# Performance work log

Measured on AMD Instinct MI355X. Metric: run time of the kernel, lower is better.

## Reference

```python
import jax, jax.numpy as jnp
import numpy as np

# ragged segment lengths (sum = 100000), 16 graphs of varying size
LENGTHS = np.array([3000, 5000, 7000, 2000, 9000, 4000, 6000, 8000,
                    1000, 10000, 5500, 6500, 7500, 4500, 9500, 11500], dtype=np.int64)

B, N, C_IN, K_DIM, Q_DIM, C_OUT = 4, 100000, 256, 64, 64, 128


def setup_inputs() -> dict:
    key = jax.random.key(0)
    ks = jax.random.split(key, 6)
    features = jax.random.normal(ks[0], (B, N, C_IN), dtype=jnp.float32)
    # linear-layer params (stored as [in, out]; torch Linear computes x @ W.T + b)
    Wk = jax.random.normal(ks[1], (C_IN, K_DIM), dtype=jnp.float32) / np.sqrt(C_IN)
    bk = jnp.zeros((K_DIM,), dtype=jnp.float32)
    Wq = jax.random.normal(ks[2], (C_IN, Q_DIM), dtype=jnp.float32) / np.sqrt(C_IN)
    bq = jnp.zeros((Q_DIM,), dtype=jnp.float32)
    Wv = jax.random.normal(ks[3], (C_IN, C_OUT), dtype=jnp.float32) / np.sqrt(C_IN)
    return {"features": features, "lengths": LENGTHS,
            "Wk": Wk, "bk": bk, "Wq": Wq, "bq": bq, "Wv": Wv}


def reference(features, lengths, Wk, bk, Wq, bq, Wv):
    # projections + (elu + 1) feature map for keys/queries
    k = jax.nn.elu(features @ Wk + bk) + 1.0   # [B, N, K]
    q = jax.nn.elu(features @ Wq + bq) + 1.0   # [B, N, Q]
    v = features @ Wv                           # [B, N, O]
    # static ragged offsets (lengths is a concrete numpy array)
    offs = np.concatenate([[0], np.cumsum(np.asarray(lengths))]).astype(np.int64)
    outs = []
    for i in range(len(offs) - 1):  # loop over fixed small set of graphs
        s, e = int(offs[i]), int(offs[i + 1])
        ktv = jnp.einsum('bnk,bno->bko', k[:, s:e], v[:, s:e])   # per-segment K^T V
        outs.append(jnp.einsum('bnq,bqo->bno', q[:, s:e], ktv))  # Q (K^T V)
    return jnp.concatenate(outs, axis=1)  # [B, N, O]
```

## Files before the change

kernel.cpp:

```cpp
#include <hip/hip_runtime.h>
#include <hip/hip_bf16.h>

#define B_ 4
#define N_ 100000

typedef unsigned short u16;
typedef unsigned int u32;
typedef __attribute__((ext_vector_type(8))) __bf16 bf16x8;
typedef __attribute__((ext_vector_type(4))) float floatx4;

__device__ const int d_OFFS[17]  = {0,3000,8000,15000,17000,26000,30000,36000,44000,45000,55000,60500,67000,74500,79000,88500,100000};
__device__ const int d_CH512[17] = {0,6,16,30,34,52,60,72,88,90,110,121,134,149,158,177,200};
__device__ const int d_CH128[17] = {0,24,64,119,135,206,238,285,348,356,435,478,529,588,624,699,789};

__device__ __forceinline__ u16 f2bf(float f) {
    union { float f; unsigned u; } x; x.f = f;
    unsigned r = x.u + 0x7fffu + ((x.u >> 16) & 1u);
    return (u16)(r >> 16);
}

union U4 { u32 u[4]; bf16x8 v; uint4 q; };

__global__ void prep_kernel(const float* __restrict__ Wk, const float* __restrict__ bk,
                            const float* __restrict__ Wq, const float* __restrict__ bq,
                            const float* __restrict__ Wv,
                            u16* __restrict__ Bt, float* __restrict__ bias) {
    int idx = blockIdx.x * 256 + threadIdx.x;
    int n = idx >> 8, kk = idx & 255;
    float w;
    if (n < 64)        w = Wk[kk*64 + n];
    else if (n < 128)  w = Wq[kk*64 + (n-64)];
    else               w = Wv[kk*128 + (n-128)];
    Bt[n*256 + kk] = f2bf(w);
    if (blockIdx.x == 0) {
        int c = threadIdx.x;
        bias[c] = (c < 64) ? bk[c] : (c < 128 ? bq[c-64] : 0.f);
    }
}

__global__ __launch_bounds__(512, 4) void proj_kernel(const float* __restrict__ feat,
        const u16* __restrict__ Bt, const float* __restrict__ bias,
        u16* __restrict__ kws, u16* __restrict__ qws, u16* __restrict__ vws) {
    __shared__ u16 ldsA[128][40];
    __shared__ u16 ldsB[256][40];
    const int t = threadIdx.x, lane = t & 63, wave = t >> 6;
    const int wrow = wave & 1, wcol = wave >> 1;
    const long row0 = (long)blockIdx.x * 128;

    floatx4 acc[4][4];
    #pragma unroll
    for (int i = 0; i < 4; ++i)
        #pragma unroll
        for (int j = 0; j < 4; ++j) acc[i][j] = (floatx4)(0.f);

    const int asr = t >> 2, ask = (t & 3) * 8;
    const int bsr = t >> 1, bsk = (t & 1) * 16;

    float4 pf0, pf1; uint4 pb0, pb1;
    {
        const float* src = feat + (row0 + asr) * 256 + ask;
        pf0 = *(const float4*)(src); pf1 = *(const float4*)(src + 4);
        const u16* bsrc = Bt + bsr*256 + bsk;
        pb0 = *(const uint4*)bsrc; pb1 = *(const uint4*)(bsrc + 8);
    }

    for (int kc = 0; kc < 8; ++kc) {
        __syncthreads();
        {
            u16 tmp[8] __attribute__((aligned(16)));
            tmp[0]=f2bf(pf0.x); tmp[1]=f2bf(pf0.y); tmp[2]=f2bf(pf0.z); tmp[3]=f2bf(pf0.w);
            tmp[4]=f2bf(pf1.x); tmp[5]=f2bf(pf1.y); tmp[6]=f2bf(pf1.z); tmp[7]=f2bf(pf1.w);
            *(uint4*)&ldsA[asr][ask] = *(const uint4*)tmp;
            *(uint4*)&ldsB[bsr][bsk]   = pb0;
            *(uint4*)&ldsB[bsr][bsk+8] = pb1;
        }
        __syncthreads();
        if (kc < 7) {
            const float* src = feat + (row0 + asr) * 256 + (kc+1)*32 + ask;
            pf0 = *(const float4*)(src); pf1 = *(const float4*)(src + 4);
            const u16* bsrc = Bt + bsr*256 + (kc+1)*32 + bsk;
            pb0 = *(const uint4*)bsrc; pb1 = *(const uint4*)(bsrc + 8);
        }
        bf16x8 af[4];
        #pragma unroll
        for (int mt = 0; mt < 4; ++mt)
            af[mt] = *(const bf16x8*)&ldsA[wrow*64 + mt*16 + (lane & 15)][(lane >> 4) * 8];
        #pragma unroll
        for (int nt = 0; nt < 4; ++nt) {
            bf16x8 bfv = *(const bf16x8*)&ldsB[wcol*64 + nt*16 + (lane & 15)][(lane >> 4) * 8];
            #pragma unroll
            for (int mt = 0; mt < 4; ++mt)
                acc[mt][nt] = __builtin_amdgcn_mfma_f32_16x16x32_bf16(af[mt], bfv, acc[mt][nt], 0, 0, 0);
        }
    }
    #pragma unroll
    for (int nt = 0; nt < 4; ++nt) {
        int col = wcol*64 + nt*16 + (lane & 15);
        float bc = (col < 128) ? bias[col] : 0.f;
        #pragma unroll
        for (int mt = 0; mt < 4; ++mt) {
            #pragma unroll
            for (int reg = 0; reg < 4; ++reg) {
                long row = row0 + wrow*64 + mt*16 + (lane >> 4)*4 + reg;
                float val = acc[mt][nt][reg] + bc;
                if (col < 64) {
                    val = (val > 0.f) ? (val + 1.f) : __expf(val);
                    kws[row*64 + col] = f2bf(val);
                } else if (col < 128) {
                    val = (val > 0.f) ? (val + 1.f) : __expf(val);
                    qws[row*64 + (col-64)] = f2bf(val);
                } else {
                    vws[row*128 + (col-128)] = f2bf(val);
                }
            }
        }
    }
}

__global__ __launch_bounds__(256) void ktvp_kernel(const u16* __restrict__ kws,
                                                   const u16* __restrict__ vws,
                                                   float* __restrict__ part) {
    __shared__ u16 Kt[64][34];
    __shared__ u16 Vt[128][34];
    const int t = threadIdx.x, lane = t & 63, mt = t >> 6;
    const int b = blockIdx.y, cid = blockIdx.x;
    int seg = 0;
    #pragma unroll
    for (int s = 0; s < 16; ++s) if (cid >= d_CH512[s+1]) seg = s + 1;
    const int n0   = d_OFFS[seg] + (cid - d_CH512[seg]) * 512;
    const int nend = d_OFFS[seg+1];

    floatx4 acc[8];
    #pragma unroll
    for (int i = 0; i < 8; ++i) acc[i] = (floatx4)(0.f);

    const int srr = t >> 3;
    const int kp  = (t & 7) * 8;
    const int op  = (t & 7) * 16;

    for (int sub = 0; sub < 16; ++sub) {
        int nb = n0 + sub * 32;
        if (nb >= nend) break;
        __syncthreads();
        int n = nb + srr;
        if (n < nend) {
            long gr = (long)b * N_ + n;
            U4 kv; kv.q = *(const uint4*)(kws + gr*64 + kp);
            const u16* k16 = (const u16*)&kv;
            #pragma unroll
            for (int j = 0; j < 8; ++j) Kt[kp+j][srr] = k16[j];
            U4 v0; v0.q = *(const uint4*)(vws + gr*128 + op);
            U4 v1; v1.q = *(const uint4*)(vws + gr*128 + op + 8);
            const u16* va = (const u16*)&v0;
            const u16* vb = (const u16*)&v1;
            #pragma unroll
            for (int j = 0; j < 8; ++j) { Vt[op+j][srr] = va[j]; Vt[op+8+j][srr] = vb[j]; }
        } else {
            #pragma unroll
            for (int j = 0; j < 8; ++j) Kt[kp+j][srr] = 0;
            #pragma unroll
            for (int j = 0; j < 16; ++j) Vt[op+j][srr] = 0;
        }
        __syncthreads();
        const int k0 = (lane >> 4) * 8;
        U4 a;
        { const u32* pa = (const u32*)&Kt[mt*16 + (lane & 15)][k0];
          a.u[0]=pa[0]; a.u[1]=pa[1]; a.u[2]=pa[2]; a.u[3]=pa[3]; }
        #pragma unroll
        for (int nt = 0; nt < 8; ++nt) {
            U4 bb;
            const u32* pb = (const u32*)&Vt[nt*16 + (lane & 15)][k0];
            bb.u[0]=pb[0]; bb.u[1]=pb[1]; bb.u[2]=pb[2]; bb.u[3]=pb[3];
            acc[nt] = __builtin_amdgcn_mfma_f32_16x16x32_bf16(a.v, bb.v, acc[nt], 0, 0, 0);
        }
    }
    float* dst = part + ((long)cid*4 + b) * 8192;
    #pragma unroll
    for (int nt = 0; nt < 8; ++nt)
        #pragma unroll
        for (int reg = 0; reg < 4; ++reg) {
            int kd = mt*16 + (lane >> 4)*4 + reg;
            dst[kd*128 + nt*16 + (lane & 15)] = acc[nt][reg];
        }
}

__global__ void reduce_kernel(const float* __restrict__ part, u16* __restrict__ ktvT) {
    int bx = blockIdx.x;
    int sb = bx >> 2, q = bx & 3;
    int seg = sb >> 2, b = sb & 3;
    int c0 = d_CH512[seg], c1 = d_CH512[seg+1];
    int t = threadIdx.x;
    #pragma unroll
    for (int i = 0; i < 8; ++i) {
        int idx = q*2048 + i*256 + t;
        float s = 0.f;
        for (int c = c0; c < c1; ++c)
            s += part[((long)c*4 + b)*8192 + idx];
        int kk = idx >> 7, o = idx & 127;
        ktvT[sb*8192 + o*64 + kk] = f2bf(s);
    }
}

__global__ __launch_bounds__(256) void out_kernel(const u16* __restrict__ qws,
                                                  const u16* __restrict__ ktvT,
                                                  float* __restrict__ out) {
    __shared__ u16 ldsA[128][72];
    __shared__ u16 ldsB[128][72];
    const int t = threadIdx.x, lane = t & 63, wave = t >> 6;
    const int wrow = wave & 1, wcol = wave >> 1;
    const int b = blockIdx.y, cid = blockIdx.x;
    int seg = 0;
    #pragma unroll
    for (int s = 0; s < 16; ++s) if (cid >= d_CH128[s+1]) seg = s + 1;
    const int n0   = d_OFFS[seg] + (cid - d_CH128[seg]) * 128;
    const int nend = d_OFFS[seg+1];
    const int sb = seg*4 + b;

    floatx4 acc[4][4];
    #pragma unroll
    for (int i = 0; i < 4; ++i)
        #pragma unroll
        for (int j = 0; j < 4; ++j) acc[i][j] = (floatx4)(0.f);

    const int sr = t >> 1, kh = (t & 1) * 32;
    {
        int n = n0 + sr;
        if (n < nend) {
            const u16* src = qws + ((long)b * N_ + n)*64 + kh;
            #pragma unroll
            for (int i = 0; i < 4; ++i)
                *(uint4*)&ldsA[sr][kh + i*8] = *(const uint4*)(src + i*8);
        } else {
            uint4 z = {0,0,0,0};
            #pragma unroll
            for (int i = 0; i < 4; ++i) *(uint4*)&ldsA[sr][kh + i*8] = z;
        }
        const u16* bsrc = ktvT + sb*8192 + sr*64 + kh;
        #pragma unroll
        for (int i = 0; i < 4; ++i)
            *(uint4*)&ldsB[sr][kh + i*8] = *(const uint4*)(bsrc + i*8);
    }
    __syncthreads();
    #pragma unroll
    for (int kc = 0; kc < 2; ++kc) {
        bf16x8 af[4];
        #pragma unroll
        for (int mt = 0; mt < 4; ++mt)
            af[mt] = *(const bf16x8*)&ldsA[wrow*64 + mt*16 + (lane & 15)][kc*32 + (lane >> 4)*8];
        #pragma unroll
        for (int nt = 0; nt < 4; ++nt) {
            bf16x8 bfv = *(const bf16x8*)&ldsB[wcol*64 + nt*16 + (lane & 15)][kc*32 + (lane >> 4)*8];
            #pragma unroll
            for (int mt = 0; mt < 4; ++mt)
                acc[mt][nt] = __builtin_amdgcn_mfma_f32_16x16x32_bf16(af[mt], bfv, acc[mt][nt], 0, 0, 0);
        }
    }
    #pragma unroll
    for (int nt = 0; nt < 4; ++nt) {
        int col = wcol*64 + nt*16 + (lane & 15);
        #pragma unroll
        for (int mt = 0; mt < 4; ++mt)
            #pragma unroll
            for (int reg = 0; reg < 4; ++reg) {
                int n = n0 + wrow*64 + mt*16 + (lane >> 4)*4 + reg;
                if (n < nend)
                    out[((long)b * N_ + n)*128 + col] = acc[mt][nt][reg];
            }
    }
}

extern "C" void kernel_launch(void* const* d_in, const int* in_sizes, int n_in,
                              void* d_out, int out_size, void* d_ws, size_t ws_size,
                              hipStream_t stream) {
    (void)in_sizes; (void)n_in; (void)out_size; (void)ws_size;
    const float* feat = (const float*)d_in[0];
    const float* Wk = (const float*)d_in[2];
    const float* bk = (const float*)d_in[3];
    const float* Wq = (const float*)d_in[4];
    const float* bq = (const float*)d_in[5];
    const float* Wv = (const float*)d_in[6];
    float* out = (float*)d_out;

    char* ws = (char*)d_ws;
    u16*   kws  = (u16*)  (ws);
    u16*   qws  = (u16*)  (ws + 51200000);
    u16*   Bt   = (u16*)  (ws + 102400000);
    float* bias = (float*)(ws + 102531072);
    u16*   ktvT = (u16*)  (ws + 102532096);

    u16*   vws  = (u16*)d_out;
    float* part = (float*)((char*)d_out + 102400000);

    prep_kernel<<<256, 256, 0, stream>>>(Wk, bk, Wq, bq, Wv, Bt, bias);
    proj_kernel<<<3125, 512, 0, stream>>>(feat, Bt, bias, kws, qws, vws);
    ktvp_kernel<<<dim3(200, 4), 256, 0, stream>>>(kws, vws, part);
    reduce_kernel<<<256, 256, 0, stream>>>(part, ktvT);
    out_kernel<<<dim3(789, 4), 256, 0, stream>>>(qws, ktvT, out);
}
```

Measured before the change: 829.7 us.

## Fuse K^T V accumulation into projection kernel with atomic fp32 reduction

The projection kernel now keeps its K and V tiles in shared memory and computes the per-segment K^T V contribution with MFMA, adding it into a float32 accumulator with atomicAdd. This removes the bf16 K/V writes to global memory, the separate ktvp and reduce kernels, and the partial buffer. The out kernel reads the fp32 K^T V and converts it to bf16 as it loads. The costs are heavy atomic traffic, about 3125 blocks × 8192 atomics each, and slower strided shared-memory transposed reads. Zeroing of the accumulator is folded into the prep kernel.

```diff
diff --git a/kernel.cpp b/kernel.cpp
--- a/kernel.cpp
+++ b/kernel.cpp
@@ -1,5 +1,4 @@
 #include <hip/hip_runtime.h>
-#include <hip/hip_bf16.h>
 
 #define B_ 4
 #define N_ 100000
@@ -10,7 +9,6 @@
 typedef __attribute__((ext_vector_type(4))) float floatx4;
 
 __device__ const int d_OFFS[17]  = {0,3000,8000,15000,17000,26000,30000,36000,44000,45000,55000,60500,67000,74500,79000,88500,100000};
-__device__ const int d_CH512[17] = {0,6,16,30,34,52,60,72,88,90,110,121,134,149,158,177,200};
 __device__ const int d_CH128[17] = {0,24,64,119,135,206,238,285,348,356,435,478,529,588,624,699,789};
 
 __device__ __forceinline__ u16 f2bf(float f) {
@@ -24,7 +22,8 @@
 __global__ void prep_kernel(const float* __restrict__ Wk, const float* __restrict__ bk,
                             const float* __restrict__ Wq, const float* __restrict__ bq,
                             const float* __restrict__ Wv,
-                            u16* __restrict__ Bt, float* __restrict__ bias) {
+                            u16* __restrict__ Bt, float* __restrict__ bias,
+                            float* __restrict__ ktvF) {
     int idx = blockIdx.x * 256 + threadIdx.x;
     int n = idx >> 8, kk = idx & 255;
     float w;
@@ -36,13 +35,20 @@
         int c = threadIdx.x;
         bias[c] = (c < 64) ? bk[c] : (c < 128 ? bq[c-64] : 0.f);
     }
+    float4 z = {0.f, 0.f, 0.f, 0.f};
+    float4* zd = (float4*)ktvF + (long)idx * 2;
+    zd[0] = z; zd[1] = z;
 }
 
 __global__ __launch_bounds__(512, 4) void proj_kernel(const float* __restrict__ feat,
         const u16* __restrict__ Bt, const float* __restrict__ bias,
-        u16* __restrict__ kws, u16* __restrict__ qws, u16* __restrict__ vws) {
-    __shared__ u16 ldsA[128][40];
-    __shared__ u16 ldsB[256][40];
+        u16* __restrict__ qws, float* __restrict__ ktvF) {
+    __shared__ __attribute__((aligned(16))) char smem[50176];
+    u16 (*ldsA)[40] = (u16(*)[40])smem;
+    u16 (*ldsB)[40] = (u16(*)[40])(smem + 10240);
+    u16 (*Kl)[66]   = (u16(*)[66])smem;
+    u16 (*Vl)[130]  = (u16(*)[130])(smem + 16896);
+
     const int t = threadIdx.x, lane = t & 63, wave = t >> 6;
     const int wrow = wave & 1, wcol = wave >> 1;
     const long row0 = (long)blockIdx.x * 128;
@@ -93,6 +99,8 @@
                 acc[mt][nt] = __builtin_amdgcn_mfma_f32_16x16x32_bf16(af[mt], bfv, acc[mt][nt], 0, 0, 0);
         }
     }
+
+    __syncthreads();
     #pragma unroll
     for (int nt = 0; nt < 4; ++nt) {
         int col = wcol*64 + nt*16 + (lane & 15);
@@ -101,108 +109,83 @@
         for (int mt = 0; mt < 4; ++mt) {
             #pragma unroll
             for (int reg = 0; reg < 4; ++reg) {
-                long row = row0 + wrow*64 + mt*16 + (lane >> 4)*4 + reg;
+                int r = wrow*64 + mt*16 + (lane >> 4)*4 + reg;
                 float val = acc[mt][nt][reg] + bc;
                 if (col < 64) {
                     val = (val > 0.f) ? (val + 1.f) : __expf(val);
-                    kws[row*64 + col] = f2bf(val);
+                    Kl[r][col] = f2bf(val);
                 } else if (col < 128) {
                     val = (val > 0.f) ? (val + 1.f) : __expf(val);
-                    qws[row*64 + (col-64)] = f2bf(val);
+                    qws[(row0 + r)*64 + (col-64)] = f2bf(val);
                 } else {
-                    vws[row*128 + (col-128)] = f2bf(val);
+                    Vl[r][col-128] = f2bf(val);
                 }
             }
         }
     }
-}
-
-__global__ __launch_bounds__(256) void ktvp_kernel(const u16* __restrict__ kws,
-                                                   const u16* __restrict__ vws,
-                                                   float* __restrict__ part) {
-    __shared__ u16 Kt[64][34];
-    __shared__ u16 Vt[128][34];
-    const int t = threadIdx.x, lane = t & 63, mt = t >> 6;
-    const int b = blockIdx.y, cid = blockIdx.x;
-    int seg = 0;
-    #pragma unroll
-    for (int s = 0; s < 16; ++s) if (cid >= d_CH512[s+1]) seg = s + 1;
-    const int n0   = d_OFFS[seg] + (cid - d_CH512[seg]) * 512;
-    const int nend = d_OFFS[seg+1];
-
-    floatx4 acc[8];
-    #pragma unroll
-    for (int i = 0; i < 8; ++i) acc[i] = (floatx4)(0.f);
-
-    const int srr = t >> 3;
-    const int kp  = (t & 7) * 8;
-    const int op  = (t & 7) * 16;
-
-    for (int sub = 0; sub < 16; ++sub) {
-        int nb = n0 + sub * 32;
-        if (nb >= nend) break;
-        __syncthreads();
-        int n = nb + srr;
-        if (n < nend) {
-            long gr = (long)b * N_ + n;
-            U4 kv; kv.q = *(const uint4*)(kws + gr*64 + kp);
-            const u16* k16 = (const u16*)&kv;
-            #pragma unroll
-            for (int j = 0; j < 8; ++j) Kt[kp+j][srr] = k16[j];
-            U4 v0; v0.q = *(const uint4*)(vws + gr*128 + op);
-            U4 v1; v1.q = *(const uint4*)(vws + gr*128 + op + 8);
-            const u16* va = (const u16*)&v0;
-            const u16* vb = (const u16*)&v1;
-            #pragma unroll
-            for (int j = 0; j < 8; ++j) { Vt[op+j][srr] = va[j]; Vt[op+8+j][srr] = vb[j]; }
-        } else {
-            #pragma unroll
-            for (int j = 0; j < 8; ++j) Kt[kp+j][srr] = 0;
-            #pragma unroll
-            for (int j = 0; j < 16; ++j) Vt[op+j][srr] = 0;
-        }
-        __syncthreads();
-        const int k0 = (lane >> 4) * 8;
-        U4 a;
-        { const u32* pa = (const u32*)&Kt[mt*16 + (lane & 15)][k0];
-          a.u[0]=pa[0]; a.u[1]=pa[1]; a.u[2]=pa[2]; a.u[3]=pa[3]; }
-        #pragma unroll
-        for (int nt = 0; nt < 8; ++nt) {
-            U4 bb;
-            const u32* pb = (const u32*)&Vt[nt*16 + (lane & 15)][k0];
-            bb.u[0]=pb[0]; bb.u[1]=pb[1]; bb.u[2]=pb[2]; bb.u[3]=pb[3];
-            acc[nt] = __builtin_amdgcn_mfma_f32_16x16x32_bf16(a.v, bb.v, acc[nt], 0, 0, 0);
-        }
-    }
-    float* dst = part + ((long)cid*4 + b) * 8192;
-    #pragma unroll
-    for (int nt = 0; nt < 8; ++nt)
-        #pragma unroll
-        for (int reg = 0; reg < 4; ++reg) {
-            int kd = mt*16 + (lane >> 4)*4 + reg;
-            dst[kd*128 + nt*16 + (lane & 15)] = acc[nt][reg];
-        }
-}
-
-__global__ void reduce_kernel(const float* __restrict__ part, u16* __restrict__ ktvT) {
-    int bx = blockIdx.x;
-    int sb = bx >> 2, q = bx & 3;
-    int seg = sb >> 2, b = sb & 3;
-    int c0 = d_CH512[seg], c1 = d_CH512[seg+1];
-    int t = threadIdx.x;
-    #pragma unroll
-    for (int i = 0; i < 8; ++i) {
-        int idx = q*2048 + i*256 + t;
-        float s = 0.f;
-        for (int c = c0; c < c1; ++c)
-            s += part[((long)c*4 + b)*8192 + idx];
-        int kk = idx >> 7, o = idx & 127;
-        ktvT[sb*8192 + o*64 + kk] = f2bf(s);
+
+    const long rlast = row0 + 127;
+    const int b0 = (int)(row0 / N_), n0r = (int)(row0 % N_);
+    const int b1 = (int)(rlast / N_), n1r = (int)(rlast % N_);
+    int s0 = 0, s1 = 0;
+    #pragma unroll
+    for (int s = 0; s < 16; ++s) {
+        if (n0r >= d_OFFS[s+1]) s0 = s + 1;
+        if (n1r >= d_OFFS[s+1]) s1 = s + 1;
+    }
+    const int id0 = s0*4 + b0, id1 = s1*4 + b1;
+    const long split = (long)b1 * N_ + d_OFFS[s1];
+    const int npass = (id0 == id1) ? 1 : 2;
+
+    __syncthreads();
+
+    const int mt2 = wave >> 1;
+    const int oq  = wave & 1;
+    const int kdr = mt2*16 + (lane & 15);
+    for (int pass = 0; pass < npass; ++pass) {
+        bf16x8 afr[4];
+        #pragma unroll
+        for (int ks = 0; ks < 4; ++ks) {
+            u16 tmp[8] __attribute__((aligned(16)));
+            #pragma unroll
+            for (int j = 0; j < 8; ++j) {
+                int nn = ks*32 + (lane >> 4)*8 + j;
+                u16 hv = Kl[nn][kdr];
+                if (npass == 2 && (((row0 + nn) >= split) != (pass == 1))) hv = 0;
+                tmp[j] = hv;
+            }
+            afr[ks] = *(const bf16x8*)tmp;
+        }
+        floatx4 kacc[4];
+        #pragma unroll
+        for (int i = 0; i < 4; ++i) kacc[i] = (floatx4)(0.f);
+        #pragma unroll
+        for (int ot = 0; ot < 4; ++ot) {
+            int o = (oq*4 + ot)*16 + (lane & 15);
+            #pragma unroll
+            for (int ks = 0; ks < 4; ++ks) {
+                u16 tmp[8] __attribute__((aligned(16)));
+                #pragma unroll
+                for (int j = 0; j < 8; ++j)
+                    tmp[j] = Vl[ks*32 + (lane >> 4)*8 + j][o];
+                kacc[ot] = __builtin_amdgcn_mfma_f32_16x16x32_bf16(afr[ks], *(const bf16x8*)tmp, kacc[ot], 0, 0, 0);
+            }
+        }
+        float* dst = ktvF + (long)(pass ? id1 : id0) * 8192;
+        #pragma unroll
+        for (int ot = 0; ot < 4; ++ot) {
+            int o = (oq*4 + ot)*16 + (lane & 15);
+            #pragma unroll
+            for (int reg = 0; reg < 4; ++reg) {
+                int kd = mt2*16 + (lane >> 4)*4 + reg;
+                atomicAdd(dst + kd*128 + o, kacc[ot][reg]);
+            }
+        }
     }
 }
 
 __global__ __launch_bounds__(256) void out_kernel(const u16* __restrict__ qws,
-                                                  const u16* __restrict__ ktvT,
+                                                  const float* __restrict__ ktvF,
                                                   float* __restrict__ out) {
     __shared__ u16 ldsA[128][72];
     __shared__ u16 ldsB[128][72];
@@ -235,10 +218,15 @@
             #pragma unroll
             for (int i = 0; i < 4; ++i) *(uint4*)&ldsA[sr][kh + i*8] = z;
         }
-        const u16* bsrc = ktvT + sb*8192 + sr*64 + kh;
-        #pragma unroll
-        for (int i = 0; i < 4; ++i)
-            *(uint4*)&ldsB[sr][kh + i*8] = *(const uint4*)(bsrc + i*8);
+        const float* bsrc = ktvF + (long)sb * 8192 + sr;
+        #pragma unroll
+        for (int i = 0; i < 4; ++i) {
+            u16 tmp[8] __attribute__((aligned(16)));
+            #pragma unroll
+            for (int j = 0; j < 8; ++j)
+                tmp[j] = f2bf(bsrc[(long)(kh + i*8 + j) * 128]);
+            *(uint4*)&ldsB[sr][kh + i*8] = *(const uint4*)tmp;
+        }
     }
     __syncthreads();
     #pragma unroll
@@ -282,18 +270,12 @@
     float* out = (float*)d_out;
 
     char* ws = (char*)d_ws;
-    u16*   kws  = (u16*)  (ws);
-    u16*   qws  = (u16*)  (ws + 51200000);
-    u16*   Bt   = (u16*)  (ws + 102400000);
-    float* bias = (float*)(ws + 102531072);
-    u16*   ktvT = (u16*)  (ws + 102532096);
-
-    u16*   vws  = (u16*)d_out;
-    float* part = (float*)((char*)d_out + 102400000);
-
-    prep_kernel<<<256, 256, 0, stream>>>(Wk, bk, Wq, bq, Wv, Bt, bias);
-    proj_kernel<<<3125, 512, 0, stream>>>(feat, Bt, bias, kws, qws, vws);
-    ktvp_kernel<<<dim3(200, 4), 256, 0, stream>>>(kws, vws, part);
-    reduce_kernel<<<256, 256, 0, stream>>>(part, ktvT);
-    out_kernel<<<dim3(789, 4), 256, 0, stream>>>(qws, ktvT, out);
-}
+    u16*   qws  = (u16*)  (ws);
+    u16*   Bt   = (u16*)  (ws + 51200000);
+    float* bias = (float*)(ws + 51331072);
+    float* ktvF = (float*)(ws + 51332096);
+
+    prep_kernel<<<256, 256, 0, stream>>>(Wk, bk, Wq, bq, Wv, Bt, bias, ktvF);
+    proj_kernel<<<3125, 512, 0, stream>>>(feat, Bt, bias, qws, ktvF);
+    out_kernel<<<dim3(789, 4), 256, 0, stream>>>(qws, ktvF, out);
+}
```

Result: faster. 744.0 us (-10.3%).
